# Optimization experiments

Hardware: AMD Instinct MI355X
Metric: run time of the kernel (lower is better)

Reference implementation:

```python
import jax, jax.numpy as jnp
import numpy as np

UNITS = 64
CHANNEL = 64
L1 = 32
L2 = 32
BATCH = 64


def setup_inputs() -> dict:
    key = jax.random.key(0)
    k1, k2, k3, k4, k5 = jax.random.split(key, 5)
    input_dim = CHANNEL + 3 * UNITS
    inputs = jax.random.normal(k1, (BATCH, CHANNEL, L1, L2), dtype=jnp.float32)
    W = jax.random.normal(k2, (input_dim, UNITS * 7), dtype=jnp.float32) * (1.0 / np.sqrt(input_dim))
    U_rec = jax.random.normal(k3, (UNITS * 3, UNITS), dtype=jnp.float32) * (1.0 / np.sqrt(UNITS * 3))
    bias = jnp.zeros((UNITS * 8,), dtype=jnp.float32)
    W_ij = jax.random.normal(k4, (CHANNEL, UNITS), dtype=jnp.float32) * (1.0 / np.sqrt(CHANNEL))
    return {"inputs": inputs, "W": W, "U_rec": U_rec, "bias": bias, "W_ij": W_ij}


def reference(inputs, W, U_rec, bias, W_ij):
    B, C, l1, l2 = inputs.shape
    u = W_ij.shape[1]
    wr, br = W[:, : 3 * u], bias[: 3 * u]
    wz, bz = W[:, 3 * u : 7 * u], bias[3 * u : 7 * u]
    b_ij = bias[7 * u :]

    # [L1*L2, B, C] scan order: row-major over (i, j), direction 'lt'
    x = jnp.transpose(inputs, (2, 3, 0, 1)).reshape(l1 * l2, B, C)
    states0 = jnp.zeros((l1 + 1, l2 + 1, B, u), dtype=inputs.dtype)  # zero boundary

    def step(carry, xs):
        states, _ = carry
        s_ij, t = xs
        i = t // l2
        j = t % l2
        h_diag = states[i, j]        # [B, u]
        h_top = states[i, j + 1]
        h_left = states[i + 1, j]
        # q = [h_top, h_left, h_diag, s_ij] : [B, 3u + C]
        q = jnp.concatenate([h_top, h_left, h_diag, s_ij], axis=1)
        r = jax.nn.sigmoid(q @ wr + br)                     # [B, 3u]
        z = q @ wz + bz                                     # [B, 4u]
        zg = jax.nn.softmax(z.reshape(B, 4, u), axis=1)     # softmax across 4 gates per unit
        zi, zl, zt, zd = zg[:, 0], zg[:, 1], zg[:, 2], zg[:, 3]
        h_hat = jnp.tanh(
            s_ij @ W_ij + b_ij
            + (r * jnp.concatenate([h_left, h_top, h_diag], axis=1)) @ U_rec
        )
        h_ij = zl * h_left + zt * h_top + zd * h_diag + zi * h_hat
        states = states.at[i + 1, j + 1].set(h_ij)
        return (states, h_ij), None

    tsteps = jnp.arange(l1 * l2)
    (_, h_last), _ = jax.lax.scan(
        step, (states0, jnp.zeros((B, u), dtype=inputs.dtype)), (x, tsteps)
    )
    return h_last
```

## Files before the change

### kernel.cpp

```cpp
#include <hip/hip_runtime.h>
#include <cstdint>
#include <cstddef>


#define LDIM   32
#define BATCH  64
#define UNITS  64
#define CHAN   64
#define NBT    4
#define BT     16
#define TPB    512

typedef _Float16 f16;
typedef _Float16 f16x8 __attribute__((ext_vector_type(8)));
typedef float    f32x4 __attribute__((ext_vector_type(4)));

__global__ __launch_bounds__(TPB, 2) void spatial_gru_kernel(
    const float* __restrict__ x,
    const float* __restrict__ W,
    const float* __restrict__ Urec,
    const float* __restrict__ bias,
    const float* __restrict__ Wij,
    float* __restrict__ out,
    uint32_t* __restrict__ hbuf)
{
    const int p    = blockIdx.x;
    const int xcd  = p & 7;
    const int slot = p >> 3;
    const int row  = xcd * 4 + (slot >> 2);
    const int bt   = slot & 3;
    const int b0   = bt * BT;
    const int t    = (int)threadIdx.x;
    const int u    = t & 63;
    const int g    = t >> 6;
    const int l15  = t & 15;
    const int lq   = (t & 63) >> 4;

    __shared__ __attribute__((aligned(16))) f16 qf[BT][328];
    __shared__ __attribute__((aligned(16))) f16 rf[BT][200];
    __shared__ float qs32[BT][324];
    __shared__ float Gsz [BT][260];

    f16x8 wreg[4][8];
    float bias1[4] = {0.f, 0.f, 0.f, 0.f};
    if (g < 7) {
        const int nb = g * 64 + l15;
#pragma unroll
        for (int T = 0; T < 4; ++T) {
            bias1[T] = bias[nb + 16 * T];
#pragma unroll
            for (int s = 0; s < 8; ++s) {
                f16x8 v;
#pragma unroll
                for (int jj = 0; jj < 8; ++jj) {
                    int kk = s * 32 + lq * 8 + jj;
                    v[jj] = (f16)W[(size_t)kk * 448 + nb + 16 * T];
                }
                wreg[T][s] = v;
            }
        }
    }
    f16x8 wreg2[8];
    float bijE = 0.f;
    if (g >= 4) {
        const int nn = (g - 4) * 16 + l15;
        bijE = bias[448 + nn];
#pragma unroll
        for (int s = 0; s < 8; ++s) {
            f16x8 v;
#pragma unroll
            for (int jj = 0; jj < 8; ++jj) {
                int kk = s * 32 + lq * 8 + jj;
                float wv = (kk < 192) ? Urec[kk * 64 + nn] : Wij[(kk - 192) * 64 + nn];
                v[jj] = (f16)wv;
            }
            wreg2[s] = v;
        }
    }

    for (int idx = t; idx < BT * 324; idx += TPB)
        ((float*)qs32)[idx] = 0.f;
    for (int idx = t; idx < 192 * BT; idx += TPB) {
        int b = idx & 15, k = idx >> 4;
        qf[b][k] = (f16)0.f;
    }

    const size_t xb0 = (size_t)(b0 + g) * 65536 + (size_t)u * 1024 + (size_t)row * 32;
    const size_t xb1 = xb0 + (size_t)8 * 65536;
    {
        float x0 = x[xb0], x1 = x[xb1];
        qf[g][192 + u]     = (f16)x0;
        qf[g + 8][192 + u] = (f16)x1;
    }

    for (int j = 0; j < LDIM; ++j) {
        const int par  = j & 1;
        const int scur = 192 + par * 64;
        const int snxt = 192 + (par ^ 1) * 64;
        const int hlc  = 64 + par * 128, hdc = 128 + par * 128;
        const int hln  = 64 + (par ^ 1) * 128, hdn = 128 + (par ^ 1) * 128;

        __syncthreads();

        uint32_t wv_ = 0;
        const uint32_t* sp = hbuf;
        if (row > 0) {
            sp = hbuf + ((((size_t)(row - 1) * LDIM + j) * NBT + bt) << 9) + (g << 6) + u;
            wv_ = __hip_atomic_load(sp, __ATOMIC_RELAXED, __HIP_MEMORY_SCOPE_AGENT);
        }
        float nx0 = 0.f, nx1 = 0.f;
        if (j < LDIM - 1) { nx0 = x[xb0 + j + 1]; nx1 = x[xb1 + j + 1]; }

        f32x4 acc[4];
        if (g < 7) {
#pragma unroll
            for (int T = 0; T < 4; ++T)
                acc[T] = (f32x4){bias1[T], bias1[T], bias1[T], bias1[T]};
#pragma unroll
            for (int s = 2; s < 8; ++s) {
                const f16* ap = (s < 6) ? &qf[l15][s * 32 + lq * 8]
                                        : &qf[l15][scur + (s - 6) * 32 + lq * 8];
                f16x8 a = *(const f16x8*)ap;
#pragma unroll
                for (int T = 0; T < 4; ++T)
                    acc[T] = __builtin_amdgcn_mfma_f32_16x16x32_f16(a, wreg[T][s], acc[T], 0, 0, 0);
            }
        }

        {
            float ht0 = 0.f, ht1 = 0.f;
            f16 hf0 = (f16)0.f, hf1 = (f16)0.f;
            if (row > 0) {
                while ((wv_ & 0x00010001u) != 0x00010001u) {
                    __builtin_amdgcn_s_sleep(1);
                    wv_ = __hip_atomic_load(sp, __ATOMIC_RELAXED, __HIP_MEMORY_SCOPE_AGENT);
                }
                uint16_t lo = (uint16_t)(wv_ & 0xFFFFu), hi = (uint16_t)(wv_ >> 16);
                hf0 = __builtin_bit_cast(f16, lo);
                hf1 = __builtin_bit_cast(f16, hi);
                ht0 = (float)hf0;
                ht1 = (float)hf1;
            }
            qs32[g][u]     = ht0;  qf[g][u]     = hf0;
            qs32[g + 8][u] = ht1;  qf[g + 8][u] = hf1;
        }
        __syncthreads();

        if (g < 7) {
            {
                f16x8 a0 = *(const f16x8*)&qf[l15][lq * 8];
                f16x8 a1 = *(const f16x8*)&qf[l15][32 + lq * 8];
#pragma unroll
                for (int T = 0; T < 4; ++T)
                    acc[T] = __builtin_amdgcn_mfma_f32_16x16x32_f16(a0, wreg[T][0], acc[T], 0, 0, 0);
#pragma unroll
                for (int T = 0; T < 4; ++T)
                    acc[T] = __builtin_amdgcn_mfma_f32_16x16x32_f16(a1, wreg[T][1], acc[T], 0, 0, 0);
            }
            if (g < 3) {
                const int colbase = (g == 0) ? hlc : (g == 1) ? 0 : hdc;
#pragma unroll
                for (int T = 0; T < 4; ++T)
#pragma unroll
                    for (int r = 0; r < 4; ++r) {
                        float rr = 1.f / (1.f + __expf(-acc[T][r]));
                        int b = lq * 4 + r;
                        float hv = qs32[b][colbase + T * 16 + l15];
                        rf[b][g * 64 + T * 16 + l15] = (f16)(rr * hv);
                    }
            } else {
                const int zb = (g - 3) * 64;
#pragma unroll
                for (int T = 0; T < 4; ++T)
#pragma unroll
                    for (int r = 0; r < 4; ++r)
                        Gsz[lq * 4 + r][zb + T * 16 + l15] = acc[T][r];
            }
        }
        __syncthreads();

        if (g >= 4) {
            f32x4 aA = (f32x4){0.f, 0.f, 0.f, 0.f};
            f32x4 aB = (f32x4){0.f, 0.f, 0.f, 0.f};
#pragma unroll
            for (int s = 0; s < 8; s += 2) {
                const f16* apA = (s < 6) ? &rf[l15][s * 32 + lq * 8]
                                         : &qf[l15][scur + (s - 6) * 32 + lq * 8];
                f16x8 a = *(const f16x8*)apA;
                aA = __builtin_amdgcn_mfma_f32_16x16x32_f16(a, wreg2[s], aA, 0, 0, 0);
                const f16* apB = (s + 1 < 6) ? &rf[l15][(s + 1) * 32 + lq * 8]
                                             : &qf[l15][scur + (s + 1 - 6) * 32 + lq * 8];
                f16x8 b_ = *(const f16x8*)apB;
                aB = __builtin_amdgcn_mfma_f32_16x16x32_f16(b_, wreg2[s + 1], aB, 0, 0, 0);
            }
            const int n = (g - 4) * 16 + l15;
            uint16_t* hp = (uint16_t*)(hbuf + ((((size_t)row * LDIM + j) * NBT + bt) << 9));
#pragma unroll
            for (int rr = 0; rr < 4; ++rr) {
                const int b = lq * 4 + rr;
                float hh = bijE + aA[rr] + aB[rr];
                float e2 = __expf(2.f * hh);
                float th = 1.f - 2.f / (e2 + 1.f);
                float zi = Gsz[b][n],       zl = Gsz[b][64 + n];
                float zt = Gsz[b][128 + n], zd = Gsz[b][192 + n];
                float hT = qs32[b][n], hL = qs32[b][hlc + n], hD = qs32[b][hdc + n];
                float mx = fmaxf(fmaxf(zi, zl), fmaxf(zt, zd));
                float ei = __expf(zi - mx), el = __expf(zl - mx);
                float et = __expf(zt - mx), ed = __expf(zd - mx);
                float inv = 1.f / (ei + el + et + ed);
                float h = (el * hL + et * hT + ed * hD + ei * th) * inv;
                uint16_t hv16 = (uint16_t)(__builtin_bit_cast(uint16_t, (f16)h) | 1u);
                __hip_atomic_store(hp + ((((b & 7) << 6) + n) << 1) + (b >> 3),
                                   hv16, __ATOMIC_RELAXED, __HIP_MEMORY_SCOPE_AGENT);
                qs32[b][hln + n] = h;
                qf[b][64 + n]    = (f16)h;
                if (row == LDIM - 1 && j == LDIM - 1)
                    out[(size_t)(b0 + b) * UNITS + n] = h;
            }
        } else {
#pragma unroll
            for (int i = 0; i < 4; ++i) {
                const int b = g + 4 * i;
                qs32[b][hdn + u] = qs32[b][u];
                qf[b][128 + u]   = qf[b][u];
            }
        }
        qf[g][snxt + u]     = (f16)nx0;
        qf[g + 8][snxt + u] = (f16)nx1;
    }
}

extern "C" void kernel_launch(void* const* d_in, const int* in_sizes, int n_in,
                              void* d_out, int out_size, void* d_ws, size_t ws_size,
                              hipStream_t stream) {
    const float* x    = (const float*)d_in[0];
    const float* W    = (const float*)d_in[1];
    const float* Urec = (const float*)d_in[2];
    const float* bias = (const float*)d_in[3];
    const float* Wij  = (const float*)d_in[4];
    float* out = (float*)d_out;

    uint32_t* hbuf = (uint32_t*)d_ws;

    spatial_gru_kernel<<<LDIM * NBT, TPB, 0, stream>>>(
        x, W, Urec, bias, Wij, out, hbuf);
}
```

Baseline: 282.6 us.

## Split gate blend across warps and publish tanh and partial sums separately

Moves the softmax-gate blend out of the four tanh waves so the other four waves compute the partial sum of the left, top and diagonal terms and the input-gate weight in parallel. When the workspace is large enough, the tanh value, partial sum and gate weight are each published to global memory as flagged fp16 words. The next row then rebuilds h as partial + weight*tanh, which takes the softmax work off the critical path between rows. The cost is three polled loads per consumer, three times the workspace traffic, and extra fp16 rounding. If the workspace is too small, it instead uses an extra block barrier to combine the pieces locally.

```diff
diff --git a/kernel.cpp b/kernel.cpp
--- a/kernel.cpp
+++ b/kernel.cpp
@@ -4,12 +4,10 @@
 
 
 #define LDIM   32
-#define BATCH  64
-#define UNITS  64
-#define CHAN   64
 #define NBT    4
 #define BT     16
 #define TPB    512
+#define UNITS  64
 
 typedef _Float16 f16;
 typedef _Float16 f16x8 __attribute__((ext_vector_type(8)));
@@ -22,7 +20,8 @@
     const float* __restrict__ bias,
     const float* __restrict__ Wij,
     float* __restrict__ out,
-    uint32_t* __restrict__ hbuf)
+    uint32_t* __restrict__ hbuf,
+    const int SPLIT)
 {
     const int p    = blockIdx.x;
     const int xcd  = p & 7;
@@ -35,6 +34,7 @@
     const int g    = t >> 6;
     const int l15  = t & 15;
     const int lq   = (t & 63) >> 4;
+    const int STR  = SPLIT ? 1536 : 512;
 
     __shared__ __attribute__((aligned(16))) f16 qf[BT][328];
     __shared__ __attribute__((aligned(16))) f16 rf[BT][200];
@@ -102,11 +102,15 @@
 
         __syncthreads();
 
-        uint32_t wv_ = 0;
+        uint32_t wT = 0, wZ = 0, wE = 0;
         const uint32_t* sp = hbuf;
         if (row > 0) {
-            sp = hbuf + ((((size_t)(row - 1) * LDIM + j) * NBT + bt) << 9) + (g << 6) + u;
-            wv_ = __hip_atomic_load(sp, __ATOMIC_RELAXED, __HIP_MEMORY_SCOPE_AGENT);
+            sp = hbuf + (size_t)(((row - 1) * LDIM + j) * NBT + bt) * STR + (g << 6) + u;
+            wT = __hip_atomic_load(sp, __ATOMIC_RELAXED, __HIP_MEMORY_SCOPE_AGENT);
+            if (SPLIT) {
+                wZ = __hip_atomic_load(sp + 512,  __ATOMIC_RELAXED, __HIP_MEMORY_SCOPE_AGENT);
+                wE = __hip_atomic_load(sp + 1024, __ATOMIC_RELAXED, __HIP_MEMORY_SCOPE_AGENT);
+            }
         }
         float nx0 = 0.f, nx1 = 0.f;
         if (j < LDIM - 1) { nx0 = x[xb0 + j + 1]; nx1 = x[xb1 + j + 1]; }
@@ -131,15 +135,33 @@
             float ht0 = 0.f, ht1 = 0.f;
             f16 hf0 = (f16)0.f, hf1 = (f16)0.f;
             if (row > 0) {
-                while ((wv_ & 0x00010001u) != 0x00010001u) {
-                    __builtin_amdgcn_s_sleep(1);
-                    wv_ = __hip_atomic_load(sp, __ATOMIC_RELAXED, __HIP_MEMORY_SCOPE_AGENT);
-                }
-                uint16_t lo = (uint16_t)(wv_ & 0xFFFFu), hi = (uint16_t)(wv_ >> 16);
-                hf0 = __builtin_bit_cast(f16, lo);
-                hf1 = __builtin_bit_cast(f16, hi);
-                ht0 = (float)hf0;
-                ht1 = (float)hf1;
+                if (SPLIT) {
+                    while (((wT & wZ & wE) & 0x00010001u) != 0x00010001u) {
+                        __builtin_amdgcn_s_sleep(1);
+                        wT = __hip_atomic_load(sp,        __ATOMIC_RELAXED, __HIP_MEMORY_SCOPE_AGENT);
+                        wZ = __hip_atomic_load(sp + 512,  __ATOMIC_RELAXED, __HIP_MEMORY_SCOPE_AGENT);
+                        wE = __hip_atomic_load(sp + 1024, __ATOMIC_RELAXED, __HIP_MEMORY_SCOPE_AGENT);
+                    }
+                    f16 th0 = __builtin_bit_cast(f16, (uint16_t)(wT & 0xFFFFu));
+                    f16 th1 = __builtin_bit_cast(f16, (uint16_t)(wT >> 16));
+                    f16 zp0 = __builtin_bit_cast(f16, (uint16_t)(wZ & 0xFFFFu));
+                    f16 zp1 = __builtin_bit_cast(f16, (uint16_t)(wZ >> 16));
+                    f16 ei0 = __builtin_bit_cast(f16, (uint16_t)(wE & 0xFFFFu));
+                    f16 ei1 = __builtin_bit_cast(f16, (uint16_t)(wE >> 16));
+                    ht0 = (float)zp0 + (float)ei0 * (float)th0;
+                    ht1 = (float)zp1 + (float)ei1 * (float)th1;
+                    hf0 = (f16)ht0;
+                    hf1 = (f16)ht1;
+                } else {
+                    while ((wT & 0x00010001u) != 0x00010001u) {
+                        __builtin_amdgcn_s_sleep(1);
+                        wT = __hip_atomic_load(sp, __ATOMIC_RELAXED, __HIP_MEMORY_SCOPE_AGENT);
+                    }
+                    hf0 = __builtin_bit_cast(f16, (uint16_t)(wT & 0xFFFFu));
+                    hf1 = __builtin_bit_cast(f16, (uint16_t)(wT >> 16));
+                    ht0 = (float)hf0;
+                    ht1 = (float)hf1;
+                }
             }
             qs32[g][u]     = ht0;  qf[g][u]     = hf0;
             qs32[g + 8][u] = ht1;  qf[g + 8][u] = hf1;
@@ -178,6 +200,10 @@
             }
         }
         __syncthreads();
+
+        const size_t curbase = (size_t)((row * LDIM + j) * NBT + bt) * STR;
+        uint16_t* hp16 = (uint16_t*)(hbuf + curbase);
+        float thv[4] = {0.f, 0.f, 0.f, 0.f};
 
         if (g >= 4) {
             f32x4 aA = (f32x4){0.f, 0.f, 0.f, 0.f};
@@ -194,39 +220,86 @@
                 aB = __builtin_amdgcn_mfma_f32_16x16x32_f16(b_, wreg2[s + 1], aB, 0, 0, 0);
             }
             const int n = (g - 4) * 16 + l15;
-            uint16_t* hp = (uint16_t*)(hbuf + ((((size_t)row * LDIM + j) * NBT + bt) << 9));
 #pragma unroll
             for (int rr = 0; rr < 4; ++rr) {
                 const int b = lq * 4 + rr;
                 float hh = bijE + aA[rr] + aB[rr];
                 float e2 = __expf(2.f * hh);
-                float th = 1.f - 2.f / (e2 + 1.f);
-                float zi = Gsz[b][n],       zl = Gsz[b][64 + n];
-                float zt = Gsz[b][128 + n], zd = Gsz[b][192 + n];
-                float hT = qs32[b][n], hL = qs32[b][hlc + n], hD = qs32[b][hdc + n];
+                thv[rr] = 1.f - 2.f / (e2 + 1.f);
+                if (SPLIT) {
+                    uint16_t th16 = (uint16_t)(__builtin_bit_cast(uint16_t, (f16)thv[rr]) | 1u);
+                    __hip_atomic_store(hp16 + ((((b & 7) << 6) + n) << 1) + (b >> 3),
+                                       th16, __ATOMIC_RELAXED, __HIP_MEMORY_SCOPE_AGENT);
+                }
+            }
+            if (SPLIT) {
+#pragma unroll
+                for (int rr = 0; rr < 4; ++rr) {
+                    const int b = lq * 4 + rr;
+                    float zi = Gsz[b][n],       zl = Gsz[b][64 + n];
+                    float zt = Gsz[b][128 + n], zd = Gsz[b][192 + n];
+                    float hT = qs32[b][n], hL = qs32[b][hlc + n], hD = qs32[b][hdc + n];
+                    float mx = fmaxf(fmaxf(zi, zl), fmaxf(zt, zd));
+                    float ei = __expf(zi - mx), el = __expf(zl - mx);
+                    float et = __expf(zt - mx), ed = __expf(zd - mx);
+                    float inv = 1.f / (ei + el + et + ed);
+                    float h = (el * hL + et * hT + ed * hD + ei * thv[rr]) * inv;
+                    qs32[b][hln + n] = h;
+                    qf[b][64 + n]    = (f16)h;
+                    if (row == LDIM - 1 && j == LDIM - 1)
+                        out[(size_t)(b0 + b) * UNITS + n] = h;
+                }
+            }
+        } else {
+#pragma unroll
+            for (int i = 0; i < 4; ++i) {
+                const int b = g * 4 + i;
+                float zi = Gsz[b][u],       zl = Gsz[b][64 + u];
+                float zt = Gsz[b][128 + u], zd = Gsz[b][192 + u];
+                float hT = qs32[b][u], hL = qs32[b][hlc + u], hD = qs32[b][hdc + u];
                 float mx = fmaxf(fmaxf(zi, zl), fmaxf(zt, zd));
                 float ei = __expf(zi - mx), el = __expf(zl - mx);
                 float et = __expf(zt - mx), ed = __expf(zd - mx);
                 float inv = 1.f / (ei + el + et + ed);
-                float h = (el * hL + et * hT + ed * hD + ei * th) * inv;
-                uint16_t hv16 = (uint16_t)(__builtin_bit_cast(uint16_t, (f16)h) | 1u);
-                __hip_atomic_store(hp + ((((b & 7) << 6) + n) << 1) + (b >> 3),
-                                   hv16, __ATOMIC_RELAXED, __HIP_MEMORY_SCOPE_AGENT);
-                qs32[b][hln + n] = h;
-                qf[b][64 + n]    = (f16)h;
-                if (row == LDIM - 1 && j == LDIM - 1)
-                    out[(size_t)(b0 + b) * UNITS + n] = h;
-            }
-        } else {
-#pragma unroll
-            for (int i = 0; i < 4; ++i) {
-                const int b = g + 4 * i;
-                qs32[b][hdn + u] = qs32[b][u];
+                float zp  = (el * hL + et * hT + ed * hD) * inv;
+                float eiv = ei * inv;
+                if (SPLIT) {
+                    uint16_t zp16 = (uint16_t)(__builtin_bit_cast(uint16_t, (f16)zp)  | 1u);
+                    uint16_t ei16 = (uint16_t)(__builtin_bit_cast(uint16_t, (f16)eiv) | 1u);
+                    const int dw = ((b & 7) << 6) + u;
+                    __hip_atomic_store(hp16 + ((512  + dw) << 1) + (b >> 3),
+                                       zp16, __ATOMIC_RELAXED, __HIP_MEMORY_SCOPE_AGENT);
+                    __hip_atomic_store(hp16 + ((1024 + dw) << 1) + (b >> 3),
+                                       ei16, __ATOMIC_RELAXED, __HIP_MEMORY_SCOPE_AGENT);
+                } else {
+                    Gsz[b][u]      = zp;
+                    Gsz[b][64 + u] = eiv;
+                }
+                qs32[b][hdn + u] = hT;
                 qf[b][128 + u]   = qf[b][u];
             }
         }
         qf[g][snxt + u]     = (f16)nx0;
         qf[g + 8][snxt + u] = (f16)nx1;
+
+        if (!SPLIT) {
+            __syncthreads();
+            if (g >= 4) {
+                const int n = (g - 4) * 16 + l15;
+#pragma unroll
+                for (int rr = 0; rr < 4; ++rr) {
+                    const int b = lq * 4 + rr;
+                    float h = Gsz[b][n] + Gsz[b][64 + n] * thv[rr];
+                    uint16_t h16 = (uint16_t)(__builtin_bit_cast(uint16_t, (f16)h) | 1u);
+                    __hip_atomic_store(hp16 + ((((b & 7) << 6) + n) << 1) + (b >> 3),
+                                       h16, __ATOMIC_RELAXED, __HIP_MEMORY_SCOPE_AGENT);
+                    qs32[b][hln + n] = h;
+                    qf[b][64 + n]    = (f16)h;
+                    if (row == LDIM - 1 && j == LDIM - 1)
+                        out[(size_t)(b0 + b) * UNITS + n] = h;
+                }
+            }
+        }
     }
 }
 
@@ -240,8 +313,10 @@
     const float* Wij  = (const float*)d_in[4];
     float* out = (float*)d_out;
 
+    const size_t need = (size_t)LDIM * LDIM * NBT * 1536 * 4;
+    const int split = (ws_size >= need) ? 1 : 0;
     uint32_t* hbuf = (uint32_t*)d_ws;
 
     spatial_gru_kernel<<<LDIM * NBT, TPB, 0, stream>>>(
-        x, W, Urec, bias, Wij, out, hbuf);
+        x, W, Urec, bias, Wij, out, hbuf, split);
 }
```

Result: no change. 284.1 us (+0.5%).

## Process four grid rows per block as an in-block wavefront with fewer batch items

Applied to the files above, without the earlier changes.

Each block now owns a group of four consecutive grid rows and only four batch elements, not one row with sixteen. The four rows run as a skewed wavefront inside the block over LDIM+3 steps, and each row's new state feeds the next row through shared memory. Cross-block global-memory flag polling happens only between row groups, cutting the number of inter-block handoffs on the critical path. The cost is three extra pipeline fill/drain steps and more, smaller blocks (8x16 instead of 32x4), each doing fewer batch items per MFMA tile row.

```diff
diff --git a/kernel.cpp b/kernel.cpp
--- a/kernel.cpp
+++ b/kernel.cpp
@@ -4,12 +4,13 @@
 
 
 #define LDIM   32
-#define BATCH  64
+#define GRPS   8
+#define RPB    4
+#define NBT    16
+#define BT     4
+#define TPB    512
 #define UNITS  64
-#define CHAN   64
-#define NBT    4
-#define BT     16
-#define TPB    512
+#define STEPS  (LDIM + RPB - 1)
 
 typedef _Float16 f16;
 typedef _Float16 f16x8 __attribute__((ext_vector_type(8)));
@@ -24,22 +25,19 @@
     float* __restrict__ out,
     uint32_t* __restrict__ hbuf)
 {
-    const int p    = blockIdx.x;
-    const int xcd  = p & 7;
-    const int slot = p >> 3;
-    const int row  = xcd * 4 + (slot >> 2);
-    const int bt   = slot & 3;
-    const int b0   = bt * BT;
-    const int t    = (int)threadIdx.x;
-    const int u    = t & 63;
-    const int g    = t >> 6;
-    const int l15  = t & 15;
-    const int lq   = (t & 63) >> 4;
-
-    __shared__ __attribute__((aligned(16))) f16 qf[BT][328];
-    __shared__ __attribute__((aligned(16))) f16 rf[BT][200];
-    __shared__ float qs32[BT][324];
-    __shared__ float Gsz [BT][260];
+    const int p   = blockIdx.x;
+    const int grp = p >> 4;
+    const int bt  = p & 15;
+    const int t   = (int)threadIdx.x;
+    const int u   = t & 63;
+    const int g   = t >> 6;
+    const int l15 = t & 15;
+    const int lq  = (t & 63) >> 4;
+
+    __shared__ __attribute__((aligned(16))) f16 qf[16][520];
+    __shared__ __attribute__((aligned(16))) f16 rf[16][200];
+    __shared__ float qs32[16][388];
+    __shared__ float Gsz [16][260];
 
     f16x8 wreg[4][8];
     float bias1[4] = {0.f, 0.f, 0.f, 0.f};
@@ -78,38 +76,49 @@
         }
     }
 
-    for (int idx = t; idx < BT * 324; idx += TPB)
-        ((float*)qs32)[idx] = 0.f;
-    for (int idx = t; idx < 192 * BT; idx += TPB) {
+    for (int idx = t; idx < 16 * 388; idx += TPB) {
+        int b = idx & 15, k = idx >> 4;
+        qs32[b][k] = 0.f;
+    }
+    for (int idx = t; idx < 16 * 384; idx += TPB) {
         int b = idx & 15, k = idx >> 4;
         qf[b][k] = (f16)0.f;
     }
 
-    const size_t xb0 = (size_t)(b0 + g) * 65536 + (size_t)u * 1024 + (size_t)row * 32;
-    const size_t xb1 = xb0 + (size_t)8 * 65536;
-    {
-        float x0 = x[xb0], x1 = x[xb1];
-        qf[g][192 + u]     = (f16)x0;
-        qf[g + 8][192 + u] = (f16)x1;
-    }
-
-    for (int j = 0; j < LDIM; ++j) {
-        const int par  = j & 1;
-        const int scur = 192 + par * 64;
-        const int snxt = 192 + (par ^ 1) * 64;
-        const int hlc  = 64 + par * 128, hdc = 128 + par * 128;
-        const int hln  = 64 + (par ^ 1) * 128, hdn = 128 + (par ^ 1) * 128;
+    const int m0 = g * 2, m1 = g * 2 + 1;
+    const size_t xb0 = ((size_t)(bt * BT + (m0 & 3)) << 16) + ((size_t)u << 10)
+                     + ((size_t)(grp * RPB + (m0 >> 2)) << 5);
+    const size_t xb1 = ((size_t)(bt * BT + (m1 & 3)) << 16) + ((size_t)u << 10)
+                     + ((size_t)(grp * RPB + (m1 >> 2)) << 5);
+    qf[m0][384 + u] = (f16)(((m0 >> 2) == 0) ? x[xb0] : 0.f);
+    qf[m1][384 + u] = (f16)(((m1 >> 2) == 0) ? x[xb1] : 0.f);
+
+    for (int s = 0; s < STEPS; ++s) {
+        const int par = s & 1;
+        const int fhT = par * 64,        nhT = (par ^ 1) * 64;
+        const int fhL = 128 + par * 64,  nhL = 128 + (par ^ 1) * 64;
+        const int fhD = 256 + par * 64,  nhD = 256 + (par ^ 1) * 64;
+        const int fx  = 384 + par * 64,  nx  = 384 + (par ^ 1) * 64;
+        const int shT = par * 64,        tnT = (par ^ 1) * 64;
+        const int shL = 128 + par * 64,  tnL = 128 + (par ^ 1) * 64;
+        const int shD = 256 + par * 64,  tnD = 256 + (par ^ 1) * 64;
 
         __syncthreads();
 
-        uint32_t wv_ = 0;
+        uint32_t wv = 0;
         const uint32_t* sp = hbuf;
-        if (row > 0) {
-            sp = hbuf + ((((size_t)(row - 1) * LDIM + j) * NBT + bt) << 9) + (g << 6) + u;
-            wv_ = __hip_atomic_load(sp, __ATOMIC_RELAXED, __HIP_MEMORY_SCOPE_AGENT);
-        }
-        float nx0 = 0.f, nx1 = 0.f;
-        if (j < LDIM - 1) { nx0 = x[xb0 + j + 1]; nx1 = x[xb1 + j + 1]; }
+        const bool polling = (grp > 0) && (s < LDIM) && (t < 128);
+        if (polling) {
+            sp = hbuf + (((size_t)((grp - 1) * LDIM + s) * NBT + bt) << 7) + t;
+            wv = __hip_atomic_load(sp, __ATOMIC_RELAXED, __HIP_MEMORY_SCOPE_AGENT);
+        }
+        float nxv0 = 0.f, nxv1 = 0.f;
+        {
+            const int col0 = s + 1 - (m0 >> 2);
+            const int col1 = s + 1 - (m1 >> 2);
+            if ((unsigned)col0 < (unsigned)LDIM) nxv0 = x[xb0 + col0];
+            if ((unsigned)col1 < (unsigned)LDIM) nxv1 = x[xb1 + col1];
+        }
 
         f32x4 acc[4];
         if (g < 7) {
@@ -117,39 +126,32 @@
             for (int T = 0; T < 4; ++T)
                 acc[T] = (f32x4){bias1[T], bias1[T], bias1[T], bias1[T]};
 #pragma unroll
-            for (int s = 2; s < 8; ++s) {
-                const f16* ap = (s < 6) ? &qf[l15][s * 32 + lq * 8]
-                                        : &qf[l15][scur + (s - 6) * 32 + lq * 8];
-                f16x8 a = *(const f16x8*)ap;
-#pragma unroll
-                for (int T = 0; T < 4; ++T)
-                    acc[T] = __builtin_amdgcn_mfma_f32_16x16x32_f16(a, wreg[T][s], acc[T], 0, 0, 0);
-            }
-        }
-
-        {
-            float ht0 = 0.f, ht1 = 0.f;
-            f16 hf0 = (f16)0.f, hf1 = (f16)0.f;
-            if (row > 0) {
-                while ((wv_ & 0x00010001u) != 0x00010001u) {
-                    __builtin_amdgcn_s_sleep(1);
-                    wv_ = __hip_atomic_load(sp, __ATOMIC_RELAXED, __HIP_MEMORY_SCOPE_AGENT);
-                }
-                uint16_t lo = (uint16_t)(wv_ & 0xFFFFu), hi = (uint16_t)(wv_ >> 16);
-                hf0 = __builtin_bit_cast(f16, lo);
-                hf1 = __builtin_bit_cast(f16, hi);
-                ht0 = (float)hf0;
-                ht1 = (float)hf1;
-            }
-            qs32[g][u]     = ht0;  qf[g][u]     = hf0;
-            qs32[g + 8][u] = ht1;  qf[g + 8][u] = hf1;
+            for (int sc = 2; sc < 8; ++sc) {
+                const int base = (sc < 4 ? fhL : sc < 6 ? fhD : fx) + (sc & 1) * 32;
+                f16x8 a = *(const f16x8*)&qf[l15][base + lq * 8];
+#pragma unroll
+                for (int T = 0; T < 4; ++T)
+                    acc[T] = __builtin_amdgcn_mfma_f32_16x16x32_f16(a, wreg[T][sc], acc[T], 0, 0, 0);
+            }
+        }
+
+        if (polling) {
+            while ((wv & 0x00010001u) != 0x00010001u) {
+                __builtin_amdgcn_s_sleep(1);
+                wv = __hip_atomic_load(sp, __ATOMIC_RELAXED, __HIP_MEMORY_SCOPE_AGENT);
+            }
+            const int uu = t >> 1, bp = (t & 1) * 2;
+            f16 lo = __builtin_bit_cast(f16, (uint16_t)(wv & 0xFFFFu));
+            f16 hi = __builtin_bit_cast(f16, (uint16_t)(wv >> 16));
+            qs32[bp][shT + uu]     = (float)lo;  qf[bp][fhT + uu]     = lo;
+            qs32[bp + 1][shT + uu] = (float)hi;  qf[bp + 1][fhT + uu] = hi;
         }
         __syncthreads();
 
         if (g < 7) {
             {
-                f16x8 a0 = *(const f16x8*)&qf[l15][lq * 8];
-                f16x8 a1 = *(const f16x8*)&qf[l15][32 + lq * 8];
+                f16x8 a0 = *(const f16x8*)&qf[l15][fhT + lq * 8];
+                f16x8 a1 = *(const f16x8*)&qf[l15][fhT + 32 + lq * 8];
 #pragma unroll
                 for (int T = 0; T < 4; ++T)
                     acc[T] = __builtin_amdgcn_mfma_f32_16x16x32_f16(a0, wreg[T][0], acc[T], 0, 0, 0);
@@ -158,15 +160,15 @@
                     acc[T] = __builtin_amdgcn_mfma_f32_16x16x32_f16(a1, wreg[T][1], acc[T], 0, 0, 0);
             }
             if (g < 3) {
-                const int colbase = (g == 0) ? hlc : (g == 1) ? 0 : hdc;
+                const int colbase = (g == 0) ? shL : (g == 1) ? shT : shD;
 #pragma unroll
                 for (int T = 0; T < 4; ++T)
 #pragma unroll
                     for (int r = 0; r < 4; ++r) {
                         float rr = 1.f / (1.f + __expf(-acc[T][r]));
                         int b = lq * 4 + r;
-                        float hv = qs32[b][colbase + T * 16 + l15];
-                        rf[b][g * 64 + T * 16 + l15] = (f16)(rr * hv);
+                        rf[b][g * 64 + T * 16 + l15] =
+                            (f16)(rr * qs32[b][colbase + T * 16 + l15]);
                     }
             } else {
                 const int zb = (g - 3) * 64;
@@ -182,51 +184,65 @@
         if (g >= 4) {
             f32x4 aA = (f32x4){0.f, 0.f, 0.f, 0.f};
             f32x4 aB = (f32x4){0.f, 0.f, 0.f, 0.f};
-#pragma unroll
-            for (int s = 0; s < 8; s += 2) {
-                const f16* apA = (s < 6) ? &rf[l15][s * 32 + lq * 8]
-                                         : &qf[l15][scur + (s - 6) * 32 + lq * 8];
-                f16x8 a = *(const f16x8*)apA;
-                aA = __builtin_amdgcn_mfma_f32_16x16x32_f16(a, wreg2[s], aA, 0, 0, 0);
-                const f16* apB = (s + 1 < 6) ? &rf[l15][(s + 1) * 32 + lq * 8]
-                                             : &qf[l15][scur + (s + 1 - 6) * 32 + lq * 8];
-                f16x8 b_ = *(const f16x8*)apB;
-                aB = __builtin_amdgcn_mfma_f32_16x16x32_f16(b_, wreg2[s + 1], aB, 0, 0, 0);
+            {
+                f16x8 a;
+                a = *(const f16x8*)&rf[l15][  0 + lq * 8]; aA = __builtin_amdgcn_mfma_f32_16x16x32_f16(a, wreg2[0], aA, 0, 0, 0);
+                a = *(const f16x8*)&rf[l15][ 32 + lq * 8]; aB = __builtin_amdgcn_mfma_f32_16x16x32_f16(a, wreg2[1], aB, 0, 0, 0);
+                a = *(const f16x8*)&rf[l15][ 64 + lq * 8]; aA = __builtin_amdgcn_mfma_f32_16x16x32_f16(a, wreg2[2], aA, 0, 0, 0);
+                a = *(const f16x8*)&rf[l15][ 96 + lq * 8]; aB = __builtin_amdgcn_mfma_f32_16x16x32_f16(a, wreg2[3], aB, 0, 0, 0);
+                a = *(const f16x8*)&rf[l15][128 + lq * 8]; aA = __builtin_amdgcn_mfma_f32_16x16x32_f16(a, wreg2[4], aA, 0, 0, 0);
+                a = *(const f16x8*)&rf[l15][160 + lq * 8]; aB = __builtin_amdgcn_mfma_f32_16x16x32_f16(a, wreg2[5], aB, 0, 0, 0);
+                a = *(const f16x8*)&qf[l15][fx + lq * 8];      aA = __builtin_amdgcn_mfma_f32_16x16x32_f16(a, wreg2[6], aA, 0, 0, 0);
+                a = *(const f16x8*)&qf[l15][fx + 32 + lq * 8]; aB = __builtin_amdgcn_mfma_f32_16x16x32_f16(a, wreg2[7], aB, 0, 0, 0);
             }
             const int n = (g - 4) * 16 + l15;
-            uint16_t* hp = (uint16_t*)(hbuf + ((((size_t)row * LDIM + j) * NBT + bt) << 9));
+            uint32_t h16[4];
 #pragma unroll
             for (int rr = 0; rr < 4; ++rr) {
                 const int b = lq * 4 + rr;
+                const int c = b >> 2;
+                const int col = s - c;
+                const bool valid = (unsigned)col < (unsigned)LDIM;
                 float hh = bijE + aA[rr] + aB[rr];
                 float e2 = __expf(2.f * hh);
                 float th = 1.f - 2.f / (e2 + 1.f);
-                float zi = Gsz[b][n],       zl = Gsz[b][64 + n];
-                float zt = Gsz[b][128 + n], zd = Gsz[b][192 + n];
-                float hT = qs32[b][n], hL = qs32[b][hlc + n], hD = qs32[b][hdc + n];
+                float zi = Gsz[b][n],        zl = Gsz[b][64 + n];
+                float zt = Gsz[b][128 + n],  zd = Gsz[b][192 + n];
+                float hT = qs32[b][shT + n], hL = qs32[b][shL + n], hD = qs32[b][shD + n];
                 float mx = fmaxf(fmaxf(zi, zl), fmaxf(zt, zd));
                 float ei = __expf(zi - mx), el = __expf(zl - mx);
                 float et = __expf(zt - mx), ed = __expf(zd - mx);
                 float inv = 1.f / (ei + el + et + ed);
-                float h = (el * hL + et * hT + ed * hD + ei * th) * inv;
-                uint16_t hv16 = (uint16_t)(__builtin_bit_cast(uint16_t, (f16)h) | 1u);
-                __hip_atomic_store(hp + ((((b & 7) << 6) + n) << 1) + (b >> 3),
-                                   hv16, __ATOMIC_RELAXED, __HIP_MEMORY_SCOPE_AGENT);
-                qs32[b][hln + n] = h;
-                qf[b][64 + n]    = (f16)h;
-                if (row == LDIM - 1 && j == LDIM - 1)
-                    out[(size_t)(b0 + b) * UNITS + n] = h;
+                float h  = (el * hL + et * hT + ed * hD + ei * th) * inv;
+                float hs = valid ? h : 0.f;
+                f16 hf = (f16)hs;
+                h16[rr] = (uint32_t)(__builtin_bit_cast(uint16_t, hf) | 1u);
+                qs32[b][tnL + n] = hs;
+                qf[b][nhL + n]   = hf;
+                if (b < 12) {
+                    qs32[b + 4][tnT + n] = hs;
+                    qf[b + 4][nhT + n]   = hf;
+                }
+                if (b >= 12 && grp == GRPS - 1 && col == LDIM - 1)
+                    out[(size_t)(bt * BT + (b & 3)) * UNITS + n] = h;
+            }
+            if (lq == 3 && grp < GRPS - 1 && (unsigned)(s - 3) < (unsigned)LDIM) {
+                uint32_t* hp = hbuf + (((size_t)(grp * LDIM + (s - 3)) * NBT + bt) << 7);
+                __hip_atomic_store(hp + n * 2,     h16[0] | (h16[1] << 16),
+                                   __ATOMIC_RELAXED, __HIP_MEMORY_SCOPE_AGENT);
+                __hip_atomic_store(hp + n * 2 + 1, h16[2] | (h16[3] << 16),
+                                   __ATOMIC_RELAXED, __HIP_MEMORY_SCOPE_AGENT);
             }
         } else {
 #pragma unroll
             for (int i = 0; i < 4; ++i) {
                 const int b = g + 4 * i;
-                qs32[b][hdn + u] = qs32[b][u];
-                qf[b][128 + u]   = qf[b][u];
-            }
-        }
-        qf[g][snxt + u]     = (f16)nx0;
-        qf[g + 8][snxt + u] = (f16)nx1;
+                qs32[b][tnD + u] = qs32[b][shT + u];
+                qf[b][nhD + u]   = qf[b][fhT + u];
+            }
+        }
+        qf[m0][nx + u] = (f16)nxv0;
+        qf[m1][nx + u] = (f16)nxv1;
     }
 }
 
@@ -242,6 +258,6 @@
 
     uint32_t* hbuf = (uint32_t*)d_ws;
 
-    spatial_gru_kernel<<<LDIM * NBT, TPB, 0, stream>>>(
+    spatial_gru_kernel<<<GRPS * NBT, TPB, 0, stream>>>(
         x, W, Urec, bias, Wij, out, hbuf);
 }
```

Measured after the change: 290.6 us. 2.8% more time.
